# Kernel optimization log

Measured on AMD Instinct MI355X. Metric: run time of the kernel, lower is better.

## Reference

```python
import jax, jax.numpy as jnp
import numpy as np

EPS_NORM = 1e-12  # F.normalize eps
EPS_LN = 1e-5     # nn.LayerNorm eps


def setup_inputs() -> dict:
    key = jax.random.key(0)
    ks = jax.random.split(key, 8)
    B, T, N, D = 16, 12, 300, 64
    feat = jax.random.normal(ks[0], (B, T, N, D), dtype=jnp.float32)
    weights = jax.random.uniform(ks[1], (D,), dtype=jnp.float32)
    sc = 1.0 / np.sqrt(D)
    w1 = jax.random.normal(ks[2], (D, D), dtype=jnp.float32) * sc
    b1 = jax.random.normal(ks[3], (D,), dtype=jnp.float32) * sc
    w2 = jax.random.normal(ks[4], (D, D), dtype=jnp.float32) * sc
    b2 = jax.random.normal(ks[5], (D,), dtype=jnp.float32) * sc
    gamma = jnp.ones((D,), dtype=jnp.float32)
    beta = jnp.zeros((D,), dtype=jnp.float32)
    return {"feat": feat, "weights": weights, "w1": w1, "b1": b1,
            "w2": w2, "b2": b2, "gamma": gamma, "beta": beta}


def _windows(x, T2):
    # x: [B,T,N,D] -> [B,T2,3N,D] where window i = concat(x[:,i], x[:,i+1], x[:,i+2]) over node dim
    B, T, N, D = x.shape
    w = jnp.stack([x[:, i:i + T2] for i in range(3)], axis=2)  # [B,T2,3,N,D]
    return w.reshape(B, T2, 3 * N, D)


def reference(feat, weights, w1, b1, w2, b2, gamma, beta):
    B, T, N, D = feat.shape
    T2 = T - 2
    # learned edge gating + L2-normalize along feature dim
    wf = feat * jax.nn.sigmoid(weights)
    nrm = jnp.sqrt(jnp.sum(wf * wf, axis=-1, keepdims=True))
    wf = wf / jnp.maximum(nrm, EPS_NORM)
    win = _windows(feat, T2)   # [B,T2,3N,D]
    wwin = _windows(wf, T2)    # [B,T2,3N,D]
    # learned adjacency: cosine-similarity gram matrix per window
    adj = jnp.einsum('btnd,btmd->btnm', wwin, wwin)  # [B,T2,3N,3N]
    # norm_adj: row normalization, zero rows stay zero
    deg = jnp.sum(adj, axis=-1, keepdims=True)
    dinv = jnp.where(deg == 0, 0.0, 1.0 / jnp.where(deg == 0, 1.0, deg))
    adj = adj * dinv
    # aggregate, keep last N rows (current timestep nodes)
    agg = jnp.einsum('btnm,btmd->btnd', adj, win)[:, :, -N:, :]  # [B,T2,N,D]
    # FFN (dropout is eval-mode identity): Linear -> ReLU -> Linear
    h = jnp.maximum(agg @ w1 + b1, 0.0) @ w2 + b2
    # residual + LayerNorm
    s = feat[:, 2:] + h
    mu = jnp.mean(s, axis=-1, keepdims=True)
    var = jnp.mean((s - mu) ** 2, axis=-1, keepdims=True)
    out = (s - mu) * jax.lax.rsqrt(var + EPS_LN) * gamma + beta
    return out  # [B, T-2, N, D]
```

## Files before the change

kernel.cpp:

```cpp
#include <hip/hip_runtime.h>
#include <math.h>

#define BB  16
#define TT  12
#define T2C 10
#define NN  300
#define DD  64
#define M3  900
#define NW  (BB*T2C)

typedef _Float16 f16;
typedef __attribute__((ext_vector_type(8)))  _Float16 f16x8;
typedef __attribute__((ext_vector_type(16))) float    f32x16;

#define KS 72

static __device__ inline unsigned pk2(f16 a, f16 b) {
    union { f16 h[2]; unsigned u; } x; x.h[0] = a; x.h[1] = b; return x.u;
}

__global__ __launch_bounds__(256) void k_prep(const float* __restrict__ feat,
                                              const float* __restrict__ weights,
                                              const float* __restrict__ w1,
                                              const float* __restrict__ w2,
                                              float* __restrict__ sigw,
                                              float* __restrict__ invn,
                                              float* __restrict__ tspart,
                                              f16* __restrict__ w1f,
                                              f16* __restrict__ w2f) {
    int blk = blockIdx.x;
    int tid = threadIdx.x;

    if (blk == BB * TT * 5) {
        if (tid < 64) sigw[tid] = 1.0f / (1.0f + expf(-weights[tid]));
        for (int p = tid; p < 1024; p += 256) {
            int lane = p & 63, s = p >> 6;
            int mat = s >> 3, loc = s & 7, ct = loc >> 2, ks = loc & 3;
            int hcol = ct * 32 + (lane & 31);
            const float* w = mat ? w2 : w1;
            f16* dst = (mat ? w2f : w1f) + ((size_t)loc * 64 + lane) * 8;
            f16x8 v;
            #pragma unroll
            for (int j = 0; j < 8; j++) {
                int d = ks * 16 + 8 * (lane >> 5) + j;
                v[j] = (f16)w[d * DD + hcol];
            }
            *(f16x8*)dst = v;
        }
        return;
    }

    __shared__ float part[4][64];
    int bt = blk / 5, ch = blk % 5;
    int row0 = bt * NN + ch * 60;
    int w = tid >> 6, lane = tid & 63;
    int r16 = lane >> 4, c4 = lane & 15;

    float4 wv = *(const float4*)(weights + c4 * 4);
    float4 sg;
    sg.x = 1.0f / (1.0f + expf(-wv.x)); sg.y = 1.0f / (1.0f + expf(-wv.y));
    sg.z = 1.0f / (1.0f + expf(-wv.z)); sg.w = 1.0f / (1.0f + expf(-wv.w));

    float ax = 0.f, ay = 0.f, az = 0.f, aw = 0.f;
    for (int g = w; g < 15; g += 4) {
        int row = row0 + g * 4 + r16;
        float4 f = *(const float4*)(feat + (size_t)row * DD + c4 * 4);
        float xx = f.x * sg.x, xy = f.y * sg.y, xz = f.z * sg.z, xw = f.w * sg.w;
        float ss = xx * xx + xy * xy + xz * xz + xw * xw;
        ss += __shfl_xor(ss, 1, 64);
        ss += __shfl_xor(ss, 2, 64);
        ss += __shfl_xor(ss, 4, 64);
        ss += __shfl_xor(ss, 8, 64);
        float in = 1.0f / fmaxf(sqrtf(ss), 1e-12f);
        if (c4 == 0) invn[row] = in;
        ax += f.x * in; ay += f.y * in; az += f.z * in; aw += f.w * in;
    }
    #pragma unroll
    for (int off = 16; off <= 32; off <<= 1) {
        ax += __shfl_xor(ax, off, 64); ay += __shfl_xor(ay, off, 64);
        az += __shfl_xor(az, off, 64); aw += __shfl_xor(aw, off, 64);
    }
    if (r16 == 0) {
        float* p = &part[w][c4 * 4];
        p[0] = ax * sg.x; p[1] = ay * sg.y; p[2] = az * sg.z; p[3] = aw * sg.w;
    }
    __syncthreads();
    if (tid < 64)
        tspart[(size_t)blk * 64 + tid] =
            part[0][tid] + part[1][tid] + part[2][tid] + part[3][tid];
}

__global__ __launch_bounds__(256) void k_M(const float* __restrict__ feat,
                                           const float* __restrict__ invn,
                                           float* __restrict__ Mt) {
    __shared__ f16 Kti[64 * KS];
    __shared__ f16 Vtt[64 * KS];
    int bt = blockIdx.x;
    int row0 = bt * NN;
    int tid = threadIdx.x;
    int wv = tid >> 6, lane = tid & 63;
    int l31 = lane & 31, lh = lane >> 5;
    int ci = wv & 1, di = wv >> 1;

    int mr = (tid & 31) * 2;
    int cb = (tid >> 5) * 8;

    f32x16 acc;
    #pragma unroll
    for (int i = 0; i < 16; i++) acc[i] = 0.f;

    for (int ep = 0; ep < 5; ep++) {
        __syncthreads();
        int gm0 = ep * 64 + mr, gm1 = gm0 + 1;
        bool ok0 = gm0 < NN, ok1 = gm1 < NN;
        int g0 = row0 + (ok0 ? gm0 : 0);
        int g1 = row0 + (ok1 ? gm1 : 0);
        float4 a0 = *(const float4*)(feat + (size_t)g0 * DD + cb);
        float4 a1 = *(const float4*)(feat + (size_t)g0 * DD + cb + 4);
        float4 b0 = *(const float4*)(feat + (size_t)g1 * DD + cb);
        float4 b1 = *(const float4*)(feat + (size_t)g1 * DD + cb + 4);
        float i0 = ok0 ? invn[g0] : 0.f;
        float i1 = ok1 ? invn[g1] : 0.f;
        float av[8] = {a0.x, a0.y, a0.z, a0.w, a1.x, a1.y, a1.z, a1.w};
        float bv[8] = {b0.x, b0.y, b0.z, b0.w, b1.x, b1.y, b1.z, b1.w};
        #pragma unroll
        for (int i = 0; i < 8; i++) {
            *(unsigned*)&Kti[(cb + i) * KS + mr] = pk2((f16)(av[i] * i0), (f16)(bv[i] * i1));
            *(unsigned*)&Vtt[(cb + i) * KS + mr] = pk2((f16)av[i], (f16)bv[i]);
        }
        __syncthreads();
        #pragma unroll
        for (int ks = 0; ks < 4; ks++) {
            f16x8 af = *(const f16x8*)&Kti[(ci * 32 + l31) * KS + ks * 16 + 8 * lh];
            f16x8 bf = *(const f16x8*)&Vtt[(di * 32 + l31) * KS + ks * 16 + 8 * lh];
            acc = __builtin_amdgcn_mfma_f32_32x32x16_f16(af, bf, acc, 0, 0, 0);
        }
    }
    float* mb = Mt + (size_t)bt * 4096;
    #pragma unroll
    for (int g = 0; g < 4; g++)
        *(float4*)&mb[(di * 32 + l31) * 64 + ci * 32 + 8 * g + 4 * lh] =
            make_float4(acc[4 * g + 0], acc[4 * g + 1], acc[4 * g + 2], acc[4 * g + 3]);
}

__global__ __launch_bounds__(256) void k_U(const float* __restrict__ feat,
                                           const float* __restrict__ sigw,
                                           const float* __restrict__ invn,
                                           const float* __restrict__ tspart,
                                           const float* __restrict__ Mt,
                                           const f16* __restrict__ w1f,
                                           const f16* __restrict__ w2f,
                                           const float* __restrict__ b1,
                                           const float* __restrict__ b2,
                                           const float* __restrict__ gamma,
                                           const float* __restrict__ beta,
                                           float* __restrict__ out) {
    __shared__ union __align__(16) {
        f16 Mh[64 * KS];
        f16 Hl[64 * KS];
    } MH;
    __shared__ float Ol[64 * 68];
    __shared__ float red[64][4][2];
    __shared__ float rmax[64][4];
    __shared__ float scls[64];
    __shared__ float isls[64];
    __shared__ float degp[64][4];
    __shared__ float degs[64];
    __shared__ float ksumL[64];

    int blk = blockIdx.x;
    int wdw = blk % NW;
    int rb  = blk / NW;
    int t2 = wdw % T2C, b = wdw / T2C;
    int n0 = rb * 64;
    int qrow0 = (b * TT + t2 + 2) * NN;
    int tid = threadIdx.x;
    int wv = tid >> 6, lane = tid & 63;
    int l31 = lane & 31, lh = lane >> 5;
    int nt = wv & 1;
    int dt = wv >> 1;
    int ct = wv & 1, rt = wv >> 1;
    int r = tid >> 2, q = tid & 3, c0 = q * 16;

    f16x8 w1a[4], w2a[4];
    #pragma unroll
    for (int ks = 0; ks < 4; ks++) {
        w1a[ks] = *(const f16x8*)(w1f + ((size_t)(ct * 4 + ks) * 64 + lane) * 8);
        w2a[ks] = *(const f16x8*)(w2f + ((size_t)(ct * 4 + ks) * 64 + lane) * 8);
    }

    if (tid < 64) {
        const float* tp = tspart + (size_t)(b * TT + t2) * 5 * 64 + tid;
        float s = 0.f;
        #pragma unroll
        for (int j = 0; j < 15; j++) s += tp[j * 64];
        ksumL[tid] = s;
    }

    f16x8 qf[4];
    {
        int nloc = n0 + nt * 32 + l31;
        bool ok = nloc < NN;
        int gr = qrow0 + (ok ? nloc : 0);
        float in = ok ? invn[gr] : 0.f;
        #pragma unroll
        for (int ks = 0; ks < 4; ks++) {
            int cc = ks * 16 + 8 * lh;
            float4 f0 = *(const float4*)(feat + (size_t)gr * DD + cc);
            float4 f1 = *(const float4*)(feat + (size_t)gr * DD + cc + 4);
            float4 s0 = *(const float4*)(sigw + cc);
            float4 s1 = *(const float4*)(sigw + cc + 4);
            f16x8 qv;
            qv[0] = (f16)(f0.x * s0.x * s0.x * in); qv[1] = (f16)(f0.y * s0.y * s0.y * in);
            qv[2] = (f16)(f0.z * s0.z * s0.z * in); qv[3] = (f16)(f0.w * s0.w * s0.w * in);
            qv[4] = (f16)(f1.x * s1.x * s1.x * in); qv[5] = (f16)(f1.y * s1.y * s1.y * in);
            qv[6] = (f16)(f1.z * s1.z * s1.z * in); qv[7] = (f16)(f1.w * s1.w * s1.w * in);
            qf[ks] = qv;
        }
    }

    float ms[16];
    {
        const float* mtb = Mt + (size_t)(b * TT + t2) * 4096 + r * 64 + c0;
        #pragma unroll
        for (int i = 0; i < 4; i++) {
            float4 m0 = *(const float4*)(mtb + 4 * i);
            float4 m1 = *(const float4*)(mtb + 4096 + 4 * i);
            float4 m2 = *(const float4*)(mtb + 8192 + 4 * i);
            ms[4*i+0] = m0.x + m1.x + m2.x; ms[4*i+1] = m0.y + m1.y + m2.y;
            ms[4*i+2] = m0.z + m1.z + m2.z; ms[4*i+3] = m0.w + m1.w + m2.w;
        }
    }

    int n = n0 + r;
    int nc = (n < NN) ? n : (NN - 1);
    size_t frow = ((size_t)qrow0 + nc) * DD;
    float fv[16];
    #pragma unroll
    for (int i = 0; i < 4; i++) {
        float4 f = *(const float4*)(feat + frow + c0 + 4 * i);
        fv[4*i+0] = f.x; fv[4*i+1] = f.y; fv[4*i+2] = f.z; fv[4*i+3] = f.w;
    }
    float invq = invn[qrow0 + nc];

    __syncthreads();

    {
        float p = 0.f;
        #pragma unroll
        for (int i = 0; i < 4; i++) {
            float4 s = *(const float4*)(sigw + c0 + 4 * i);
            float4 k = *(const float4*)(ksumL + c0 + 4 * i);
            p += fv[4*i+0] * s.x * k.x + fv[4*i+1] * s.y * k.y
               + fv[4*i+2] * s.z * k.z + fv[4*i+3] * s.w * k.w;
        }
        degp[r][q] = p * invq;
    }

    #pragma unroll
    for (int hhalf = 0; hhalf < 2; hhalf++) {
        f16x8 v;
        #pragma unroll
        for (int j = 0; j < 8; j++) v[j] = (f16)ms[8 * hhalf + j];
        *(f16x8*)&MH.Mh[r * KS + c0 + 8 * hhalf] = v;
    }
    __syncthreads();

    if (tid < 64)
        degs[tid] = degp[tid][0] + degp[tid][1] + degp[tid][2] + degp[tid][3];

    f32x16 ua;
    #pragma unroll
    for (int i = 0; i < 16; i++) ua[i] = 0.f;
    #pragma unroll
    for (int ks = 0; ks < 4; ks++) {
        f16x8 af = *(const f16x8*)&MH.Mh[(dt * 32 + l31) * KS + ks * 16 + 8 * lh];
        ua = __builtin_amdgcn_mfma_f32_32x32x16_f16(af, qf[ks], ua, 0, 0, 0);
    }
    __syncthreads();

    {
        int nl = nt * 32 + l31;
        float dg = degs[nl];
        float dinv = (dg == 0.f) ? 0.f : 1.f / dg;
        #pragma unroll
        for (int g = 0; g < 4; g++)
            *(float4*)&Ol[nl * 68 + dt * 32 + 8 * g + 4 * lh] =
                make_float4(ua[4*g+0] * dinv, ua[4*g+1] * dinv,
                            ua[4*g+2] * dinv, ua[4*g+3] * dinv);
    }
    __syncthreads();

    {
        float mx = 0.f;
        #pragma unroll
        for (int i = 0; i < 16; i += 4) {
            float4 f = *(const float4*)&Ol[r * 68 + c0 + i];
            mx = fmaxf(mx, fmaxf(fmaxf(fabsf(f.x), fabsf(f.y)),
                                 fmaxf(fabsf(f.z), fabsf(f.w))));
        }
        rmax[r][q] = mx;
    }
    __syncthreads();
    if (q == 0) {
        float rm = fmaxf(fmaxf(rmax[r][0], rmax[r][1]),
                         fmaxf(rmax[r][2], rmax[r][3]));
        int e = 0;
        frexpf(rm, &e);
        scls[r] = (rm > 1.f) ? exp2f((float)-e) : 1.f;
        isls[r] = (rm > 1.f) ? exp2f((float)e) : 1.f;
    }
    __syncthreads();

    float sclrow = scls[rt * 32 + l31];
    f32x16 hc;
    #pragma unroll
    for (int i = 0; i < 16; i++) hc[i] = 0.f;
    #pragma unroll
    for (int ks = 0; ks < 4; ks++) {
        const float* prw = &Ol[(rt * 32 + l31) * 68 + ks * 16 + 8 * lh];
        float4 pa = *(const float4*)prw;
        float4 pb = *(const float4*)(prw + 4);
        f16x8 bf;
        bf[0] = (f16)(pa.x * sclrow); bf[1] = (f16)(pa.y * sclrow);
        bf[2] = (f16)(pa.z * sclrow); bf[3] = (f16)(pa.w * sclrow);
        bf[4] = (f16)(pb.x * sclrow); bf[5] = (f16)(pb.y * sclrow);
        bf[6] = (f16)(pb.z * sclrow); bf[7] = (f16)(pb.w * sclrow);
        hc = __builtin_amdgcn_mfma_f32_32x32x16_f16(w1a[ks], bf, hc, 0, 0, 0);
    }
    #pragma unroll
    for (int g = 0; g < 4; g++) {
        union { f16 h[4]; uint2 u; } p;
        #pragma unroll
        for (int i = 0; i < 4; i++) {
            int hcol = ct * 32 + 8 * g + 4 * lh + i;
            p.h[i] = (f16)fmaxf(hc[4 * g + i] + sclrow * b1[hcol], 0.f);
        }
        *(uint2*)&MH.Hl[(rt * 32 + l31) * KS + ct * 32 + 8 * g + 4 * lh] = p.u;
    }
    __syncthreads();

    f32x16 oc;
    #pragma unroll
    for (int i = 0; i < 16; i++) oc[i] = 0.f;
    #pragma unroll
    for (int ks = 0; ks < 4; ks++) {
        f16x8 bf = *(const f16x8*)&MH.Hl[(rt * 32 + l31) * KS + ks * 16 + 8 * lh];
        oc = __builtin_amdgcn_mfma_f32_32x32x16_f16(w2a[ks], bf, oc, 0, 0, 0);
    }
    __syncthreads();
    #pragma unroll
    for (int g = 0; g < 4; g++) {
        float4 o4 = make_float4(oc[4*g+0], oc[4*g+1], oc[4*g+2], oc[4*g+3]);
        *(float4*)&Ol[(rt * 32 + l31) * 68 + ct * 32 + 8 * g + 4 * lh] = o4;
    }
    __syncthreads();

    float is = isls[r];
    float v[16];
    float sum = 0.f;
    #pragma unroll
    for (int i = 0; i < 16; i++) {
        int c = c0 + i;
        float x = Ol[r * 68 + c] * is + b2[c] + fv[i];
        v[i] = x; sum += x;
    }
    red[r][q][0] = sum;
    __syncthreads();
    float mu = (red[r][0][0] + red[r][1][0] + red[r][2][0] + red[r][3][0]) * (1.f / 64.f);
    float s2 = 0.f;
    #pragma unroll
    for (int i = 0; i < 16; i++) { float d = v[i] - mu; s2 += d * d; }
    red[r][q][1] = s2;
    __syncthreads();
    float var = (red[r][0][1] + red[r][1][1] + red[r][2][1] + red[r][3][1]) * (1.f / 64.f);
    float rs = rsqrtf(var + 1e-5f);
    if (n < NN) {
        size_t grow = (size_t)wdw * NN + n;
        #pragma unroll
        for (int i4 = 0; i4 < 4; i4++) {
            int c = c0 + 4 * i4;
            float4 g4 = *(const float4*)(gamma + c);
            float4 be = *(const float4*)(beta + c);
            float4 o4;
            o4.x = (v[4*i4+0] - mu) * rs * g4.x + be.x;
            o4.y = (v[4*i4+1] - mu) * rs * g4.y + be.y;
            o4.z = (v[4*i4+2] - mu) * rs * g4.z + be.z;
            o4.w = (v[4*i4+3] - mu) * rs * g4.w + be.w;
            *(float4*)(out + grow * DD + c) = o4;
        }
    }
}

extern "C" void kernel_launch(void* const* d_in, const int* in_sizes, int n_in,
                              void* d_out, int out_size, void* d_ws, size_t ws_size,
                              hipStream_t stream) {
    const float* feat    = (const float*)d_in[0];
    const float* weights = (const float*)d_in[1];
    const float* w1      = (const float*)d_in[2];
    const float* b1      = (const float*)d_in[3];
    const float* w2      = (const float*)d_in[4];
    const float* b2      = (const float*)d_in[5];
    const float* gamma   = (const float*)d_in[6];
    const float* beta    = (const float*)d_in[7];
    float* out = (float*)d_out;

    float* sigw   = (float*)d_ws;
    float* invn   = sigw + 64;
    float* tspart = invn + BB * TT * NN;
    f16*   w1f    = (f16*)(tspart + 960 * 64);
    f16*   w2f    = w1f + 4096;
    float* Mt     = (float*)(w2f + 4096);

    k_prep<<<BB * TT * 5 + 1, 256, 0, stream>>>(feat, weights, w1, w2,
                                                sigw, invn, tspart, w1f, w2f);
    k_M<<<BB * TT, 256, 0, stream>>>(feat, invn, Mt);
    k_U<<<NW * 5, 256, 0, stream>>>(feat, sigw, invn, tspart, Mt, w1f, w2f,
                                    b1, b2, gamma, beta, out);
}
```

Measured before the change: 106.7 us.

## Fuse prep normalization pass into M-matrix kernel, dropping one launch

Merges the row L2-normalization and per-timestep column-sum pass into the kernel that builds the per-timestep K^T V matrix, so feat is read once for both and one kernel launch disappears. Row inverse norms are now computed in-block through a shared-memory reduction with two extra barriers per chunk. The per-timestep sums are reduced in-kernel, so the update kernel reads three values instead of fifteen partials. The trade-off is fewer blocks (193 vs 961) for the norm work and more synchronization in the M kernel.

Result: faster. 102.4 us (-4.1%).

```diff
diff --git a/kernel.cpp b/kernel.cpp
--- a/kernel.cpp
+++ b/kernel.cpp
@@ -19,19 +19,20 @@
     union { f16 h[2]; unsigned u; } x; x.h[0] = a; x.h[1] = b; return x.u;
 }
 
-__global__ __launch_bounds__(256) void k_prep(const float* __restrict__ feat,
-                                              const float* __restrict__ weights,
-                                              const float* __restrict__ w1,
-                                              const float* __restrict__ w2,
-                                              float* __restrict__ sigw,
-                                              float* __restrict__ invn,
-                                              float* __restrict__ tspart,
-                                              f16* __restrict__ w1f,
-                                              f16* __restrict__ w2f) {
+__global__ __launch_bounds__(256) void k_pm(const float* __restrict__ feat,
+                                            const float* __restrict__ weights,
+                                            const float* __restrict__ w1,
+                                            const float* __restrict__ w2,
+                                            float* __restrict__ sigw,
+                                            float* __restrict__ invn,
+                                            float* __restrict__ tsum,
+                                            f16* __restrict__ w1f,
+                                            f16* __restrict__ w2f,
+                                            float* __restrict__ Mt) {
     int blk = blockIdx.x;
     int tid = threadIdx.x;
 
-    if (blk == BB * TT * 5) {
+    if (blk == BB * TT) {
         if (tid < 64) sigw[tid] = 1.0f / (1.0f + expf(-weights[tid]));
         for (int p = tid; p < 1024; p += 256) {
             int lane = p & 63, s = p >> 6;
@@ -50,61 +51,33 @@
         return;
     }
 
-    __shared__ float part[4][64];
-    int bt = blk / 5, ch = blk % 5;
-    int row0 = bt * NN + ch * 60;
-    int w = tid >> 6, lane = tid & 63;
-    int r16 = lane >> 4, c4 = lane & 15;
-
-    float4 wv = *(const float4*)(weights + c4 * 4);
-    float4 sg;
-    sg.x = 1.0f / (1.0f + expf(-wv.x)); sg.y = 1.0f / (1.0f + expf(-wv.y));
-    sg.z = 1.0f / (1.0f + expf(-wv.z)); sg.w = 1.0f / (1.0f + expf(-wv.w));
-
-    float ax = 0.f, ay = 0.f, az = 0.f, aw = 0.f;
-    for (int g = w; g < 15; g += 4) {
-        int row = row0 + g * 4 + r16;
-        float4 f = *(const float4*)(feat + (size_t)row * DD + c4 * 4);
-        float xx = f.x * sg.x, xy = f.y * sg.y, xz = f.z * sg.z, xw = f.w * sg.w;
-        float ss = xx * xx + xy * xy + xz * xz + xw * xw;
-        ss += __shfl_xor(ss, 1, 64);
-        ss += __shfl_xor(ss, 2, 64);
-        ss += __shfl_xor(ss, 4, 64);
-        ss += __shfl_xor(ss, 8, 64);
-        float in = 1.0f / fmaxf(sqrtf(ss), 1e-12f);
-        if (c4 == 0) invn[row] = in;
-        ax += f.x * in; ay += f.y * in; az += f.z * in; aw += f.w * in;
-    }
-    #pragma unroll
-    for (int off = 16; off <= 32; off <<= 1) {
-        ax += __shfl_xor(ax, off, 64); ay += __shfl_xor(ay, off, 64);
-        az += __shfl_xor(az, off, 64); aw += __shfl_xor(aw, off, 64);
-    }
-    if (r16 == 0) {
-        float* p = &part[w][c4 * 4];
-        p[0] = ax * sg.x; p[1] = ay * sg.y; p[2] = az * sg.z; p[3] = aw * sg.w;
-    }
-    __syncthreads();
-    if (tid < 64)
-        tspart[(size_t)blk * 64 + tid] =
-            part[0][tid] + part[1][tid] + part[2][tid] + part[3][tid];
-}
-
-__global__ __launch_bounds__(256) void k_M(const float* __restrict__ feat,
-                                           const float* __restrict__ invn,
-                                           float* __restrict__ Mt) {
     __shared__ f16 Kti[64 * KS];
     __shared__ f16 Vtt[64 * KS];
-    int bt = blockIdx.x;
+    __shared__ float sspart[64][8];
+    __shared__ float invrow[64];
+    __shared__ float tspp[32][64];
+
+    int bt = blk;
     int row0 = bt * NN;
-    int tid = threadIdx.x;
     int wv = tid >> 6, lane = tid & 63;
     int l31 = lane & 31, lh = lane >> 5;
     int ci = wv & 1, di = wv >> 1;
-
     int mr = (tid & 31) * 2;
     int cb = (tid >> 5) * 8;
 
+    float sg[8];
+    {
+        float4 wv0 = *(const float4*)(weights + cb);
+        float4 wv1 = *(const float4*)(weights + cb + 4);
+        sg[0] = 1.f/(1.f+expf(-wv0.x)); sg[1] = 1.f/(1.f+expf(-wv0.y));
+        sg[2] = 1.f/(1.f+expf(-wv0.z)); sg[3] = 1.f/(1.f+expf(-wv0.w));
+        sg[4] = 1.f/(1.f+expf(-wv1.x)); sg[5] = 1.f/(1.f+expf(-wv1.y));
+        sg[6] = 1.f/(1.f+expf(-wv1.z)); sg[7] = 1.f/(1.f+expf(-wv1.w));
+    }
+
+    float tacc[8];
+    #pragma unroll
+    for (int i = 0; i < 8; i++) tacc[i] = 0.f;
     f32x16 acc;
     #pragma unroll
     for (int i = 0; i < 16; i++) acc[i] = 0.f;
@@ -119,14 +92,34 @@
         float4 a1 = *(const float4*)(feat + (size_t)g0 * DD + cb + 4);
         float4 b0 = *(const float4*)(feat + (size_t)g1 * DD + cb);
         float4 b1 = *(const float4*)(feat + (size_t)g1 * DD + cb + 4);
-        float i0 = ok0 ? invn[g0] : 0.f;
-        float i1 = ok1 ? invn[g1] : 0.f;
         float av[8] = {a0.x, a0.y, a0.z, a0.w, a1.x, a1.y, a1.z, a1.w};
         float bv[8] = {b0.x, b0.y, b0.z, b0.w, b1.x, b1.y, b1.z, b1.w};
+
+        float ss0 = 0.f, ss1 = 0.f;
+        #pragma unroll
+        for (int i = 0; i < 8; i++) {
+            float xa = av[i] * sg[i], xb = bv[i] * sg[i];
+            ss0 += xa * xa; ss1 += xb * xb;
+        }
+        sspart[mr][tid >> 5] = ss0;
+        sspart[mr + 1][tid >> 5] = ss1;
+        __syncthreads();
+        if (tid < 64) {
+            float s = sspart[tid][0] + sspart[tid][1] + sspart[tid][2] + sspart[tid][3]
+                    + sspart[tid][4] + sspart[tid][5] + sspart[tid][6] + sspart[tid][7];
+            float in = 1.0f / fmaxf(sqrtf(s), 1e-12f);
+            invrow[tid] = in;
+            int grow = ep * 64 + tid;
+            if (grow < NN) invn[row0 + grow] = in;
+        }
+        __syncthreads();
+        float i0 = ok0 ? invrow[mr] : 0.f;
+        float i1 = ok1 ? invrow[mr + 1] : 0.f;
         #pragma unroll
         for (int i = 0; i < 8; i++) {
             *(unsigned*)&Kti[(cb + i) * KS + mr] = pk2((f16)(av[i] * i0), (f16)(bv[i] * i1));
             *(unsigned*)&Vtt[(cb + i) * KS + mr] = pk2((f16)av[i], (f16)bv[i]);
+            tacc[i] += av[i] * i0 + bv[i] * i1;
         }
         __syncthreads();
         #pragma unroll
@@ -136,17 +129,28 @@
             acc = __builtin_amdgcn_mfma_f32_32x32x16_f16(af, bf, acc, 0, 0, 0);
         }
     }
+
     float* mb = Mt + (size_t)bt * 4096;
     #pragma unroll
     for (int g = 0; g < 4; g++)
         *(float4*)&mb[(di * 32 + l31) * 64 + ci * 32 + 8 * g + 4 * lh] =
             make_float4(acc[4 * g + 0], acc[4 * g + 1], acc[4 * g + 2], acc[4 * g + 3]);
+
+    #pragma unroll
+    for (int i = 0; i < 8; i++) tspp[tid & 31][cb + i] = tacc[i] * sg[i];
+    __syncthreads();
+    if (tid < 64) {
+        float s = 0.f;
+        #pragma unroll
+        for (int g = 0; g < 32; g++) s += tspp[g][tid];
+        tsum[(size_t)bt * 64 + tid] = s;
+    }
 }
 
 __global__ __launch_bounds__(256) void k_U(const float* __restrict__ feat,
                                            const float* __restrict__ sigw,
                                            const float* __restrict__ invn,
-                                           const float* __restrict__ tspart,
+                                           const float* __restrict__ tsum,
                                            const float* __restrict__ Mt,
                                            const f16* __restrict__ w1f,
                                            const f16* __restrict__ w2f,
@@ -190,11 +194,8 @@
     }
 
     if (tid < 64) {
-        const float* tp = tspart + (size_t)(b * TT + t2) * 5 * 64 + tid;
-        float s = 0.f;
-        #pragma unroll
-        for (int j = 0; j < 15; j++) s += tp[j * 64];
-        ksumL[tid] = s;
+        const float* tp = tsum + (size_t)(b * TT + t2) * 64 + tid;
+        ksumL[tid] = tp[0] + tp[64] + tp[128];
     }
 
     f16x8 qf[4];
@@ -405,16 +406,15 @@
     const float* beta    = (const float*)d_in[7];
     float* out = (float*)d_out;
 
-    float* sigw   = (float*)d_ws;
-    float* invn   = sigw + 64;
-    float* tspart = invn + BB * TT * NN;
-    f16*   w1f    = (f16*)(tspart + 960 * 64);
-    f16*   w2f    = w1f + 4096;
-    float* Mt     = (float*)(w2f + 4096);
-
-    k_prep<<<BB * TT * 5 + 1, 256, 0, stream>>>(feat, weights, w1, w2,
-                                                sigw, invn, tspart, w1f, w2f);
-    k_M<<<BB * TT, 256, 0, stream>>>(feat, invn, Mt);
-    k_U<<<NW * 5, 256, 0, stream>>>(feat, sigw, invn, tspart, Mt, w1f, w2f,
+    float* sigw = (float*)d_ws;
+    float* invn = sigw + 64;
+    float* tsum = invn + BB * TT * NN;
+    f16*   w1f  = (f16*)(tsum + BB * TT * DD);
+    f16*   w2f  = w1f + 4096;
+    float* Mt   = (float*)(w2f + 4096);
+
+    k_pm<<<BB * TT + 1, 256, 0, stream>>>(feat, weights, w1, w2, sigw, invn,
+                                          tsum, w1f, w2f, Mt);
+    k_U<<<NW * 5, 256, 0, stream>>>(feat, sigw, invn, tsum, Mt, w1f, w2f,
                                     b1, b2, gamma, beta, out);
 }
```
